# Kernel tuning notes

Hardware: AMD Instinct MI355X
Metric: run time of the kernel (lower is better)

Reference implementation:

```python
import jax, jax.numpy as jnp
import numpy as np

DIM = 512
HEADS = 8
ALPHA = 0.5
HIDDEN = int(DIM * 2.0)
EPS = 1e-5


def _layernorm(x, g, b):
    mu = jnp.mean(x, axis=-1, keepdims=True)
    var = jnp.var(x, axis=-1, keepdims=True)
    return (x - mu) * jax.lax.rsqrt(var + EPS) * g + b


def setup_inputs() -> dict:
    key = jax.random.key(0)
    ks = jax.random.split(key, 8)
    B, N, C = 4, 1536, DIM
    s = lambda fan_in: 1.0 / np.sqrt(fan_in)
    return {
        "x": jax.random.normal(ks[0], (B, N, C), dtype=jnp.float32),
        "ln1_g": jnp.ones((C,), jnp.float32),
        "ln1_b": jnp.zeros((C,), jnp.float32),
        "qkv_w": jax.random.normal(ks[1], (C, 3 * C), jnp.float32) * s(C),
        "qkv_b": jnp.zeros((3 * C,), jnp.float32),
        "ln2_g": jnp.ones((C,), jnp.float32),
        "ln2_b": jnp.zeros((C,), jnp.float32),
        "fc1_w": jax.random.normal(ks[2], (C, HIDDEN), jnp.float32) * s(C),
        "fc1_b": jnp.zeros((HIDDEN,), jnp.float32),
        "fc2_w": jax.random.normal(ks[3], (HIDDEN, C), jnp.float32) * s(HIDDEN),
        "fc2_b": jnp.zeros((C,), jnp.float32),
    }


def reference(x, ln1_g, ln1_b, qkv_w, qkv_b, ln2_g, ln2_b, fc1_w, fc1_b, fc2_w, fc2_b):
    B, N, C = x.shape
    H = HEADS
    d = C // H
    S = N // 3

    h = _layernorm(x, ln1_g, ln1_b)
    qkv = (h @ qkv_w + qkv_b).reshape(B, N, 3, H, d)
    qkv = jnp.transpose(qkv, (2, 0, 3, 1, 4))  # [3,B,H,N,d]
    q, k, v = qkv[0], qkv[1], qkv[2]

    attn = jnp.einsum('bhnd,bhmd->bhnm', q, k) * (d ** -0.5)  # [B,H,N,N]
    # sequential cross-segment score mixing (matches in-place torch semantics)
    s0 = attn[:, :, 0:S]
    s1 = attn[:, :, S:2 * S] + ALPHA * s0
    s2 = attn[:, :, 2 * S:] + ALPHA * s1
    attn = jnp.concatenate([s0, s1, s2], axis=2)
    attn = jax.nn.softmax(attn, axis=-1)

    o = jnp.einsum('bhnm,bhmd->bhnd', attn, v)
    o = jnp.transpose(o, (0, 2, 1, 3)).reshape(B, N, C)
    x = x + o  # NOTE: self.proj is defined but unused in the original forward

    h2 = _layernorm(x, ln2_g, ln2_b)
    m = jax.nn.gelu(h2 @ fc1_w + fc1_b, approximate=False) @ fc2_w + fc2_b
    return x + m
```

## Files before the change

kernel.cpp:

```cpp
#include <hip/hip_runtime.h>
#include <hip/hip_bf16.h>
#include <math.h>

#define DIMC 512
#define NSEQ 1536
#define BATCH 4
#define NHEADS 8
#define HDIM 64
#define SSEG 512
#define HIDDEN_DIM 1024
#define ALPHA_C 0.5f
#define EPS_C 1e-5f
#define NROWS (BATCH*NSEQ)
#define SHIFT_L2 8.65617025f
#define QSCALE_L2 0.18033688f

typedef __attribute__((ext_vector_type(8))) short bfrag8;
typedef __attribute__((ext_vector_type(8))) _Float16 hfrag8;
typedef __attribute__((ext_vector_type(2))) __fp16 h2;
typedef __attribute__((ext_vector_type(4))) float ffrag;
typedef float4 f4;

__device__ __forceinline__ ushort f2bf(float v) {
    __hip_bfloat16 hb = __float2bfloat16(v);
    return *(ushort*)&hb;
}

__device__ __forceinline__ void gl2lds16(const ushort* g, ushort* l) {
    __builtin_amdgcn_global_load_lds(
        (const __attribute__((address_space(1))) unsigned*)g,
        (__attribute__((address_space(3))) unsigned*)l, 16, 0, 0);
}

__global__ __launch_bounds__(256)
void prep_kernel(const float* __restrict__ qkv_w, const float* __restrict__ fc1_w,
                 const float* __restrict__ fc2_w, ushort* __restrict__ qkv_wt,
                 ushort* __restrict__ fc1_wt, ushort* __restrict__ fc2_wt,
                 const float* __restrict__ x, const float* __restrict__ g,
                 const float* __restrict__ bvec, ushort* __restrict__ h_out)
{
    int bid = blockIdx.x;
    if (bid < 448) {
        __shared__ float tile[64][65];
        const float* W; ushort* Wt; int K, N, n0, k0;
        if (bid < 192)      { W = qkv_w; Wt = qkv_wt; K = 512;  N = 1536; int b = bid;       n0 = (b % 24) * 64; k0 = (b / 24) * 64; }
        else if (bid < 320) { W = fc1_w; Wt = fc1_wt; K = 512;  N = 1024; int b = bid - 192; n0 = (b % 16) * 64; k0 = (b / 16) * 64; }
        else                { W = fc2_w; Wt = fc2_wt; K = 1024; N = 512;  int b = bid - 320; n0 = (b % 8)  * 64; k0 = (b / 8)  * 64; }
        int tx = threadIdx.x & 63, ty = threadIdx.x >> 6;
        #pragma unroll
        for (int i = 0; i < 16; i++) {
            int r = i * 4 + ty;
            tile[r][tx] = W[(size_t)(k0 + r) * N + n0 + tx];
        }
        __syncthreads();
        #pragma unroll
        for (int i = 0; i < 16; i++) {
            int r = i * 4 + ty;
            Wt[(size_t)(n0 + r) * K + k0 + tx] = f2bf(tile[tx][r]);
        }
    } else {
        __shared__ float red[16];
        int row = bid - 448;
        int t = threadIdx.x;
        int lane = t & 63, w = t >> 6;
        const float* rp = x + (size_t)row * DIMC;
        float v0 = rp[t];
        float v1 = rp[t + 256];
        float s = v0 + v1;
        float s2 = v0 * v0 + v1 * v1;
        #pragma unroll
        for (int o = 32; o > 0; o >>= 1) {
            s  += __shfl_down(s,  o, 64);
            s2 += __shfl_down(s2, o, 64);
        }
        if (lane == 0) { red[w] = s; red[8 + w] = s2; }
        __syncthreads();
        if (t == 0) {
            float a = red[0] + red[1] + red[2] + red[3];
            float c = red[8] + red[9] + red[10] + red[11];
            red[0] = a; red[8] = c;
        }
        __syncthreads();
        float mean = red[0] * (1.0f / DIMC);
        float var  = red[8] * (1.0f / DIMC) - mean * mean;
        float rstd = rsqrtf(var + EPS_C);
        ushort* op = h_out + (size_t)row * DIMC;
        op[t]       = f2bf((v0 - mean) * rstd * g[t]       + bvec[t]);
        op[t + 256] = f2bf((v1 - mean) * rstd * g[t + 256] + bvec[t + 256]);
    }
}

__global__ __launch_bounds__(256)
void ln_kernel(const float* __restrict__ in, const float* __restrict__ g,
               const float* __restrict__ b, ushort* __restrict__ out)
{
    __shared__ float red[16];
    int row = blockIdx.x;
    int t = threadIdx.x;
    int lane = t & 63, w = t >> 6;
    const float* rp = in + (size_t)row * DIMC;
    float v0 = rp[t];
    float v1 = rp[t + 256];
    float s = v0 + v1;
    float s2 = v0 * v0 + v1 * v1;
    #pragma unroll
    for (int o = 32; o > 0; o >>= 1) {
        s  += __shfl_down(s,  o, 64);
        s2 += __shfl_down(s2, o, 64);
    }
    if (lane == 0) { red[w] = s; red[8 + w] = s2; }
    __syncthreads();
    if (t == 0) {
        float a = red[0] + red[1] + red[2] + red[3];
        float c = red[8] + red[9] + red[10] + red[11];
        red[0] = a; red[8] = c;
    }
    __syncthreads();
    float mean = red[0] * (1.0f / DIMC);
    float var  = red[8] * (1.0f / DIMC) - mean * mean;
    float rstd = rsqrtf(var + EPS_C);
    ushort* op = out + (size_t)row * DIMC;
    op[t]       = f2bf((v0 - mean) * rstd * g[t]       + b[t]);
    op[t + 256] = f2bf((v1 - mean) * rstd * g[t + 256] + b[t + 256]);
}

template <int EPI>
__device__ __forceinline__
void mgemm_body(const ushort* __restrict__ A, const ushort* __restrict__ Wt,
                const float* __restrict__ bias, const float* resid,
                void* out, int M, int K, int Nn, int bx, int by,
                ushort* As, ushort* Bs)
{
    int tid = threadIdx.x;
    int lane = tid & 63, w = tid >> 6;
    int cl = lane & 15, qg = lane >> 4;
    int wm = w >> 1, wn = w & 1;
    int rowBase = by * 64, colBase = bx * 64;
    int sr = lane >> 2;
    int sb = (lane & 3) * 8;

    const ushort* agb = A  + (size_t)(rowBase + w * 16 + sr) * K + sb;
    const ushort* bgb = Wt + (size_t)(colBase + w * 16 + sr) * K + sb;

    ffrag acc[2][2];
    #pragma unroll
    for (int mi = 0; mi < 2; mi++)
        #pragma unroll
        for (int ni = 0; ni < 2; ni++)
            #pragma unroll
            for (int r = 0; r < 4; r++) acc[mi][ni][r] = 0.f;

    int niter = K >> 6;

    #pragma unroll
    for (int hf = 0; hf < 2; hf++) {
        gl2lds16(agb + hf * 32, As + (0 * 2 + hf) * 2048 + (w * 16) * 32);
        gl2lds16(bgb + hf * 32, Bs + (0 * 2 + hf) * 2048 + (w * 16) * 32);
    }
    __syncthreads();

    for (int it = 0; it < niter; it++) {
        int cur = it & 1;
        if (it + 1 < niter) {
            int k0 = (it + 1) * 64;
            #pragma unroll
            for (int hf = 0; hf < 2; hf++) {
                gl2lds16(agb + k0 + hf * 32, As + ((cur ^ 1) * 2 + hf) * 2048 + (w * 16) * 32);
                gl2lds16(bgb + k0 + hf * 32, Bs + ((cur ^ 1) * 2 + hf) * 2048 + (w * 16) * 32);
            }
        }
        #pragma unroll
        for (int ks = 0; ks < 2; ks++) {
            bfrag8 af[2], bf[2];
            #pragma unroll
            for (int mi = 0; mi < 2; mi++)
                af[mi] = *(const bfrag8*)&As[(cur * 2 + ks) * 2048 + (wm * 32 + mi * 16 + cl) * 32 + qg * 8];
            #pragma unroll
            for (int ni = 0; ni < 2; ni++)
                bf[ni] = *(const bfrag8*)&Bs[(cur * 2 + ks) * 2048 + (wn * 32 + ni * 16 + cl) * 32 + qg * 8];
            #pragma unroll
            for (int mi = 0; mi < 2; mi++)
                #pragma unroll
                for (int ni = 0; ni < 2; ni++)
                    acc[mi][ni] = __builtin_amdgcn_mfma_f32_16x16x32_bf16(af[mi], bf[ni], acc[mi][ni], 0, 0, 0);
        }
        if (it + 1 < niter) __syncthreads();
    }

    #pragma unroll
    for (int mi = 0; mi < 2; mi++) {
        #pragma unroll
        for (int ni = 0; ni < 2; ni++) {
            #pragma unroll
            for (int r = 0; r < 4; r++) {
                int row = rowBase + wm * 32 + mi * 16 + qg * 4 + r;
                int col = colBase + wn * 32 + ni * 16 + cl;
                float v = acc[mi][ni][r] + (EPI == 3 ? bias[row] : bias[col]);
                if (EPI == 0 && col < DIMC) v *= QSCALE_L2;
                if (EPI == 1) v = 0.5f * v * (1.0f + erff(v * 0.70710678118654752f));
                if (EPI == 2) {
                    v += resid[(size_t)row * Nn + col];
                    ((float*)out)[(size_t)row * Nn + col] = v;
                } else if (EPI == 3) {
                    _Float16 e = (_Float16)v;
                    int t = col & 31;
                    int pcol = (col & ~31) | (((t & 15) >> 2) * 8 + (t >> 4) * 4 + (t & 3));
                    ((ushort*)out)[(size_t)row * Nn + pcol] = *(ushort*)&e;
                } else {
                    ((ushort*)out)[(size_t)row * Nn + col] = f2bf(v);
                }
            }
        }
    }
}

template <int EPI>
__device__ __forceinline__
void mgemm128_body(const ushort* __restrict__ A, const ushort* __restrict__ Wt,
                   const float* __restrict__ bias, void* out,
                   int K, int Nn, int bx, int by,
                   ushort* As, ushort* Bs)
{
    int tid = threadIdx.x;
    int lane = tid & 63, w = tid >> 6;
    int cl = lane & 15, qg = lane >> 4;
    int wm = w >> 1, wn = w & 1;
    int rowBase = by * 64, colBase = bx * 128;
    int sr = lane >> 2;
    int sb = (lane & 3) * 8;

    const ushort* agb = A  + (size_t)(rowBase + w * 16 + sr) * K + sb;
    const ushort* bgb = Wt + (size_t)(colBase + w * 32 + sr) * K + sb;

    ffrag acc[2][4];
    #pragma unroll
    for (int mi = 0; mi < 2; mi++)
        #pragma unroll
        for (int ni = 0; ni < 4; ni++)
            #pragma unroll
            for (int r = 0; r < 4; r++) acc[mi][ni][r] = 0.f;

    int niter = K >> 6;

    #pragma unroll
    for (int hf = 0; hf < 2; hf++) {
        gl2lds16(agb + hf * 32,                  As + (0 * 2 + hf) * 2048 + (w * 16) * 32);
        gl2lds16(bgb + hf * 32,                  Bs + (0 * 2 + hf) * 4096 + (w * 32) * 32);
        gl2lds16(bgb + (size_t)16 * K + hf * 32, Bs + (0 * 2 + hf) * 4096 + (w * 32 + 16) * 32);
    }
    __syncthreads();

    for (int it = 0; it < niter; it++) {
        int cur = it & 1;
        if (it + 1 < niter) {
            int k0 = (it + 1) * 64;
            #pragma unroll
            for (int hf = 0; hf < 2; hf++) {
                gl2lds16(agb + k0 + hf * 32,                  As + ((cur ^ 1) * 2 + hf) * 2048 + (w * 16) * 32);
                gl2lds16(bgb + k0 + hf * 32,                  Bs + ((cur ^ 1) * 2 + hf) * 4096 + (w * 32) * 32);
                gl2lds16(bgb + (size_t)16 * K + k0 + hf * 32, Bs + ((cur ^ 1) * 2 + hf) * 4096 + (w * 32 + 16) * 32);
            }
        }
        #pragma unroll
        for (int ks = 0; ks < 2; ks++) {
            bfrag8 af[2], bf[4];
            #pragma unroll
            for (int mi = 0; mi < 2; mi++)
                af[mi] = *(const bfrag8*)&As[(cur * 2 + ks) * 2048 + (wm * 32 + mi * 16 + cl) * 32 + qg * 8];
            #pragma unroll
            for (int ni = 0; ni < 4; ni++)
                bf[ni] = *(const bfrag8*)&Bs[(cur * 2 + ks) * 4096 + (wn * 64 + ni * 16 + cl) * 32 + qg * 8];
            #pragma unroll
            for (int mi = 0; mi < 2; mi++)
                #pragma unroll
                for (int ni = 0; ni < 4; ni++)
                    acc[mi][ni] = __builtin_amdgcn_mfma_f32_16x16x32_bf16(af[mi], bf[ni], acc[mi][ni], 0, 0, 0);
        }
        if (it + 1 < niter) __syncthreads();
    }

    #pragma unroll
    for (int mi = 0; mi < 2; mi++) {
        #pragma unroll
        for (int ni = 0; ni < 4; ni++) {
            #pragma unroll
            for (int r = 0; r < 4; r++) {
                int row = rowBase + wm * 32 + mi * 16 + qg * 4 + r;
                int col = colBase + wn * 64 + ni * 16 + cl;
                float v = acc[mi][ni][r] + bias[col];
                if (EPI == 0 && col < DIMC) v *= QSCALE_L2;
                if (EPI == 1) v = 0.5f * v * (1.0f + erff(v * 0.70710678118654752f));
                ((ushort*)out)[(size_t)row * Nn + col] = f2bf(v);
            }
        }
    }
}

template <int EPI>
__global__ __launch_bounds__(256)
void mgemm_kernel(const ushort* __restrict__ A, const ushort* __restrict__ Wt,
                  const float* __restrict__ bias, const float* resid,
                  void* out, int M, int K, int Nn)
{
    __shared__ ushort As[2 * 2 * 64 * 32];
    __shared__ ushort Bs[2 * 2 * 64 * 32];
    mgemm_body<EPI>(A, Wt, bias, resid, out, M, K, Nn, blockIdx.x, blockIdx.y, As, Bs);
}

template <int EPI>
__global__ __launch_bounds__(256)
void mgemm128_kernel(const ushort* __restrict__ A, const ushort* __restrict__ Wt,
                     const float* __restrict__ bias, void* out, int K, int Nn)
{
    __shared__ ushort As[2 * 2 * 64 * 32];
    __shared__ ushort Bs[2 * 2 * 128 * 32];
    mgemm128_body<EPI>(A, Wt, bias, out, K, Nn, blockIdx.x, blockIdx.y, As, Bs);
}

__global__ __launch_bounds__(256)
void qkvt_kernel(const ushort* __restrict__ h_bf, const ushort* __restrict__ qkv_wt,
                 const float* __restrict__ qkv_b, ushort* __restrict__ qkb,
                 ushort* __restrict__ vtb)
{
    __shared__ ushort smem[2 * 2 * 192 * 32];
    int bid = blockIdx.x;
    if (bid < 768) {
        mgemm128_body<0>(h_bf, qkv_wt, qkv_b, (void*)qkb,
                         DIMC, 2 * DIMC, bid & 7, bid >> 3,
                         smem, smem + 2 * 2 * 64 * 32);
    } else {
        int b2 = bid - 768;
        mgemm_body<3>(qkv_wt + (size_t)2 * DIMC * DIMC, h_bf, qkv_b + 2 * DIMC, nullptr,
                      (void*)vtb, DIMC, DIMC, NROWS, b2 % 96, b2 / 96,
                      smem, smem + 2 * 2 * 64 * 32);
    }
}

__global__ __launch_bounds__(256)
void attn_kernel(const ushort* __restrict__ qk, const ushort* __restrict__ vt,
                 const float* __restrict__ x, float* __restrict__ xres)
{
    __shared__ float Op[48][68];
    __shared__ float Lp[4][4][16][3];

    int n = blockIdx.x + (blockIdx.y << 5);
    int idx = n >> 3;
    int bh  = (n & 7) * 4 + (idx & 3);
    int qi0 = (idx >> 2) * 16;
    int b = bh >> 3, h = bh & 7;
    int tid = threadIdx.x;
    int lane = tid & 63, w = tid >> 6;
    int cl = lane & 15, qg = lane >> 4;

    const ushort* base = qk + (size_t)b * NSEQ * 1024 + h * HDIM;
    const _Float16* vbase = (const _Float16*)vt + (size_t)(h * HDIM) * NROWS + b * NSEQ;

    bfrag8 bq[3][2];
    #pragma unroll
    for (int seg = 0; seg < 3; seg++)
        #pragma unroll
        for (int f = 0; f < 2; f++)
            bq[seg][f] = *(const bfrag8*)(base + (size_t)(seg * SSEG + qi0 + cl) * 1024 + f * 32 + qg * 8);

    ffrag o[3][4];
    #pragma unroll
    for (int seg = 0; seg < 3; seg++)
        #pragma unroll
        for (int mg = 0; mg < 4; mg++)
            #pragma unroll
            for (int r = 0; r < 4; r++) o[seg][mg][r] = 0.f;
    float lp[3] = {0.f, 0.f, 0.f};

    int kb = w * 384;

    const _Float16* vp[4];
    #pragma unroll
    for (int mg = 0; mg < 4; mg++)
        vp[mg] = vbase + (size_t)(mg * 16 + cl) * NROWS + kb + qg * 8;
    const ushort* kp[2][2];
    #pragma unroll
    for (int s = 0; s < 2; s++)
        #pragma unroll
        for (int f = 0; f < 2; f++)
            kp[s][f] = base + (size_t)(kb + s * 16 + cl) * 1024 + 512 + f * 32 + qg * 8;

    auto loadf = [&](hfrag8* av, bfrag8 (*af)[2]) {
        #pragma unroll
        for (int mg = 0; mg < 4; mg++) {
            av[mg] = *(const hfrag8*)vp[mg];
            vp[mg] += 32;
        }
        #pragma unroll
        for (int s = 0; s < 2; s++)
            #pragma unroll
            for (int f = 0; f < 2; f++) {
                af[s][f] = *(const bfrag8*)kp[s][f];
                kp[s][f] += 32 * 1024;
            }
    };

    auto comp = [&](const hfrag8* av, const bfrag8 (*af)[2]) {
        ffrag c[2][3];
        #pragma unroll
        for (int s = 0; s < 2; s++) {
            #pragma unroll
            for (int seg = 0; seg < 3; seg++) {
                #pragma unroll
                for (int r = 0; r < 4; r++) c[s][seg][r] = 0.f;
                c[s][seg] = __builtin_amdgcn_mfma_f32_16x16x32_bf16(af[s][0], bq[seg][0], c[s][seg], 0, 0, 0);
                c[s][seg] = __builtin_amdgcn_mfma_f32_16x16x32_bf16(af[s][1], bq[seg][1], c[s][seg], 0, 0, 0);
            }
        }
        #pragma unroll
        for (int s = 0; s < 2; s++) {
            #pragma unroll
            for (int r = 0; r < 4; r++) {
                float s0 = c[s][0][r];
                float s1 = c[s][1][r] + ALPHA_C * s0;
                float s2 = c[s][2][r] + ALPHA_C * s1;
                float e0 = __builtin_amdgcn_exp2f(s0 - SHIFT_L2);
                float e1 = __builtin_amdgcn_exp2f(s1 - SHIFT_L2);
                float e2 = __builtin_amdgcn_exp2f(s2 - SHIFT_L2);
                c[s][0][r] = e0; c[s][1][r] = e1; c[s][2][r] = e2;
                lp[0] += e0; lp[1] += e1; lp[2] += e2;
            }
        }
        #pragma unroll
        for (int seg = 0; seg < 3; seg++) {
            union { hfrag8 v8; h2 v2[4]; } u;
            u.v2[0] = __builtin_amdgcn_cvt_pkrtz(c[0][seg][0], c[0][seg][1]);
            u.v2[1] = __builtin_amdgcn_cvt_pkrtz(c[0][seg][2], c[0][seg][3]);
            u.v2[2] = __builtin_amdgcn_cvt_pkrtz(c[1][seg][0], c[1][seg][1]);
            u.v2[3] = __builtin_amdgcn_cvt_pkrtz(c[1][seg][2], c[1][seg][3]);
            #pragma unroll
            for (int mg = 0; mg < 4; mg++)
                o[seg][mg] = __builtin_amdgcn_mfma_f32_16x16x32_f16(av[mg], u.v8, o[seg][mg], 0, 0, 0);
        }
    };

    hfrag8 avA[4], avB[4];
    bfrag8 afA[2][2], afB[2][2];
    loadf(avA, afA);
    #pragma unroll 1
    for (int it = 0; it < 12; it += 2) {
        loadf(avB, afB);
        comp(avA, afA);
        if (it + 2 < 12) loadf(avA, afA);
        comp(avB, afB);
    }

    #pragma unroll
    for (int seg = 0; seg < 3; seg++) Lp[w][qg][cl][seg] = lp[seg];

    #pragma unroll 1
    for (int wv = 0; wv < 4; wv++) {
        __syncthreads();
        if (w == wv) {
            #pragma unroll
            for (int seg = 0; seg < 3; seg++)
                #pragma unroll
                for (int mg = 0; mg < 4; mg++) {
                    float* dst = &Op[seg * 16 + cl][mg * 16 + qg * 4];
                    if (wv == 0) {
                        #pragma unroll
                        for (int r = 0; r < 4; r++) dst[r] = o[seg][mg][r];
                    } else {
                        #pragma unroll
                        for (int r = 0; r < 4; r++) dst[r] += o[seg][mg][r];
                    }
                }
        }
    }
    __syncthreads();

    if (tid < 192) {
        int row = tid >> 2;
        int seg = row >> 4, q16 = row & 15;
        int d0 = (tid & 3) * 16;
        float l = 0.f;
        #pragma unroll
        for (int wv = 0; wv < 4; wv++)
            #pragma unroll
            for (int g2 = 0; g2 < 4; g2++)
                l += Lp[wv][g2][q16][seg];
        float invl = 1.0f / l;
        size_t rowg = ((size_t)(b * NSEQ + seg * SSEG + qi0 + q16)) * DIMC + h * HDIM + d0;
        #pragma unroll
        for (int dd = 0; dd < 16; dd += 4) {
            f4 xv = *(const f4*)(x + rowg + dd);
            f4 ov;
            ov.x = Op[row][d0 + dd + 0] * invl + xv.x;
            ov.y = Op[row][d0 + dd + 1] * invl + xv.y;
            ov.z = Op[row][d0 + dd + 2] * invl + xv.z;
            ov.w = Op[row][d0 + dd + 3] * invl + xv.w;
            *(f4*)(xres + rowg + dd) = ov;
        }
    }
}

extern "C" void kernel_launch(void* const* d_in, const int* in_sizes, int n_in,
                              void* d_out, int out_size, void* d_ws, size_t ws_size,
                              hipStream_t stream)
{
    const float* x     = (const float*)d_in[0];
    const float* ln1_g = (const float*)d_in[1];
    const float* ln1_b = (const float*)d_in[2];
    const float* qkv_w = (const float*)d_in[3];
    const float* qkv_b = (const float*)d_in[4];
    const float* ln2_g = (const float*)d_in[5];
    const float* ln2_b = (const float*)d_in[6];
    const float* fc1_w = (const float*)d_in[7];
    const float* fc1_b = (const float*)d_in[8];
    const float* fc2_w = (const float*)d_in[9];
    const float* fc2_b = (const float*)d_in[10];
    float* out = (float*)d_out;

    char* p = (char*)d_ws;
    ushort* h_bf    = (ushort*)p;  p += (size_t)NROWS * DIMC * 2;
    ushort* qkb     = (ushort*)p;  p += (size_t)NROWS * 2 * DIMC * 2;
    ushort* vtb     = (ushort*)p;  p += (size_t)DIMC * NROWS * 2;
    ushort* mid     = (ushort*)p;  p += (size_t)NROWS * HIDDEN_DIM * 2;
    ushort* qkv_wt  = (ushort*)p;  p += (size_t)3 * DIMC * DIMC * 2;
    ushort* fc1_wt  = (ushort*)p;  p += (size_t)HIDDEN_DIM * DIMC * 2;
    ushort* fc2_wt  = (ushort*)p;
    float* xres = out;

    prep_kernel<<<448 + NROWS, 256, 0, stream>>>(qkv_w, fc1_w, fc2_w, qkv_wt, fc1_wt, fc2_wt,
                                                 x, ln1_g, ln1_b, h_bf);

    qkvt_kernel<<<1536, 256, 0, stream>>>(h_bf, qkv_wt, qkv_b, qkb, vtb);

    attn_kernel<<<dim3(SSEG / 16, BATCH * NHEADS), 256, 0, stream>>>(qkb, vtb, x, xres);

    ln_kernel<<<NROWS, 256, 0, stream>>>(xres, ln2_g, ln2_b, h_bf);

    mgemm128_kernel<1><<<dim3(HIDDEN_DIM / 128, NROWS / 64), 256, 0, stream>>>(
        h_bf, fc1_wt, fc1_b, (void*)mid, DIMC, HIDDEN_DIM);

    mgemm_kernel<2><<<dim3(DIMC / 64, NROWS / 64), 256, 0, stream>>>(
        mid, fc2_wt, fc2_b, xres, (void*)out, NROWS, HIDDEN_DIM, DIMC);
}
```

Baseline: 210.2 us.

## Store Q, K, V in fragment-packed per-head tiles for contiguous attention loads

The QKV GEMM epilogue now scatters Q, K and V into per-(batch,head) blocked layouts that match the MFMA fragment order. The attention kernel then reads each fragment from contiguous 1-2 KB chunks instead of strided rows 1024 or NROWS elements apart. This is meant to cut memory transactions and TLB/cache pressure in the attention inner loop. In exchange, the GEMM epilogue writes become more scattered, and address arithmetic is added on both sides.

```diff
diff --git a/kernel.cpp b/kernel.cpp
--- a/kernel.cpp
+++ b/kernel.cpp
@@ -21,6 +21,7 @@
 typedef __attribute__((ext_vector_type(4))) float ffrag;
 typedef float4 f4;
 
+
 __device__ __forceinline__ ushort f2bf(float v) {
     __hip_bfloat16 hb = __float2bfloat16(v);
     return *(ushort*)&hb;
@@ -187,6 +188,8 @@
         if (it + 1 < niter) __syncthreads();
     }
 
+    int bb = (EPI == 3) ? (colBase / 1536) : 0;
+
     #pragma unroll
     for (int mi = 0; mi < 2; mi++) {
         #pragma unroll
@@ -202,10 +205,14 @@
                     v += resid[(size_t)row * Nn + col];
                     ((float*)out)[(size_t)row * Nn + col] = v;
                 } else if (EPI == 3) {
+                    int t = col - bb * 1536;
+                    int h = row >> 6, dl = row & 63;
+                    int t32 = t & 31;
+                    int slot = ((t32 & 15) >> 2) * 8 + (t32 >> 4) * 4 + (t32 & 3);
+                    size_t a = ((size_t)(bb * 8 + h) * 48 + (t >> 5)) * 2048
+                             + (dl >> 4) * 512 + (dl & 15) * 32 + slot;
                     _Float16 e = (_Float16)v;
-                    int t = col & 31;
-                    int pcol = (col & ~31) | (((t & 15) >> 2) * 8 + (t >> 4) * 4 + (t & 3));
-                    ((ushort*)out)[(size_t)row * Nn + pcol] = *(ushort*)&e;
+                    ((ushort*)out)[a] = *(ushort*)&e;
                 } else {
                     ((ushort*)out)[(size_t)row * Nn + col] = f2bf(v);
                 }
@@ -217,7 +224,7 @@
 template <int EPI>
 __device__ __forceinline__
 void mgemm128_body(const ushort* __restrict__ A, const ushort* __restrict__ Wt,
-                   const float* __restrict__ bias, void* out,
+                   const float* __restrict__ bias, void* out, void* out2,
                    int K, int Nn, int bx, int by,
                    ushort* As, ushort* Bs)
 {
@@ -279,6 +286,8 @@
         if (it + 1 < niter) __syncthreads();
     }
 
+    int bb = (EPI == 4) ? (rowBase / 1536) : 0;
+
     #pragma unroll
     for (int mi = 0; mi < 2; mi++) {
         #pragma unroll
@@ -288,9 +297,22 @@
                 int row = rowBase + wm * 32 + mi * 16 + qg * 4 + r;
                 int col = colBase + wn * 64 + ni * 16 + cl;
                 float v = acc[mi][ni][r] + bias[col];
-                if (EPI == 0 && col < DIMC) v *= QSCALE_L2;
-                if (EPI == 1) v = 0.5f * v * (1.0f + erff(v * 0.70710678118654752f));
-                ((ushort*)out)[(size_t)row * Nn + col] = f2bf(v);
+                if (EPI == 1) {
+                    v = 0.5f * v * (1.0f + erff(v * 0.70710678118654752f));
+                    ((ushort*)out)[(size_t)row * Nn + col] = f2bf(v);
+                } else if (EPI == 4) {
+                    int t = row - bb * 1536;
+                    int h = (col >> 6) & 7;
+                    int d = col & 63;
+                    size_t a = ((size_t)(bb * 8 + h) * 96 + (t >> 4)) * 1024
+                             + (d >> 5) * 512 + (t & 15) * 32 + (d & 31);
+                    if (col < DIMC) {
+                        v *= QSCALE_L2;
+                        ((ushort*)out)[a] = f2bf(v);
+                    } else {
+                        ((ushort*)out2)[a] = f2bf(v);
+                    }
+                }
             }
         }
     }
@@ -314,30 +336,31 @@
 {
     __shared__ ushort As[2 * 2 * 64 * 32];
     __shared__ ushort Bs[2 * 2 * 128 * 32];
-    mgemm128_body<EPI>(A, Wt, bias, out, K, Nn, blockIdx.x, blockIdx.y, As, Bs);
+    mgemm128_body<EPI>(A, Wt, bias, out, nullptr, K, Nn, blockIdx.x, blockIdx.y, As, Bs);
 }
 
 __global__ __launch_bounds__(256)
 void qkvt_kernel(const ushort* __restrict__ h_bf, const ushort* __restrict__ qkv_wt,
-                 const float* __restrict__ qkv_b, ushort* __restrict__ qkb,
-                 ushort* __restrict__ vtb)
+                 const float* __restrict__ qkv_b, ushort* __restrict__ qpk,
+                 ushort* __restrict__ kpk, ushort* __restrict__ vpk)
 {
     __shared__ ushort smem[2 * 2 * 192 * 32];
     int bid = blockIdx.x;
     if (bid < 768) {
-        mgemm128_body<0>(h_bf, qkv_wt, qkv_b, (void*)qkb,
+        mgemm128_body<4>(h_bf, qkv_wt, qkv_b, (void*)qpk, (void*)kpk,
                          DIMC, 2 * DIMC, bid & 7, bid >> 3,
                          smem, smem + 2 * 2 * 64 * 32);
     } else {
         int b2 = bid - 768;
         mgemm_body<3>(qkv_wt + (size_t)2 * DIMC * DIMC, h_bf, qkv_b + 2 * DIMC, nullptr,
-                      (void*)vtb, DIMC, DIMC, NROWS, b2 % 96, b2 / 96,
+                      (void*)vpk, DIMC, DIMC, NROWS, b2 % 96, b2 / 96,
                       smem, smem + 2 * 2 * 64 * 32);
     }
 }
 
 __global__ __launch_bounds__(256)
-void attn_kernel(const ushort* __restrict__ qk, const ushort* __restrict__ vt,
+void attn_kernel(const ushort* __restrict__ qpk, const ushort* __restrict__ kpk,
+                 const ushort* __restrict__ vpk,
                  const float* __restrict__ x, float* __restrict__ xres)
 {
     __shared__ float Op[48][68];
@@ -352,15 +375,17 @@
     int lane = tid & 63, w = tid >> 6;
     int cl = lane & 15, qg = lane >> 4;
 
-    const ushort* base = qk + (size_t)b * NSEQ * 1024 + h * HDIM;
-    const _Float16* vbase = (const _Float16*)vt + (size_t)(h * HDIM) * NROWS + b * NSEQ;
+    int lofs = cl * 32 + qg * 8;
+    const ushort* qb = qpk + (size_t)bh * 96 * 1024;
+    const ushort* kb = kpk + (size_t)bh * 96 * 1024;
+    const ushort* vb = vpk + (size_t)bh * 48 * 2048;
 
     bfrag8 bq[3][2];
     #pragma unroll
     for (int seg = 0; seg < 3; seg++)
         #pragma unroll
         for (int f = 0; f < 2; f++)
-            bq[seg][f] = *(const bfrag8*)(base + (size_t)(seg * SSEG + qi0 + cl) * 1024 + f * 32 + qg * 8);
+            bq[seg][f] = *(const bfrag8*)&qb[(size_t)((seg * SSEG + qi0) >> 4) * 1024 + f * 512 + lofs];
 
     ffrag o[3][4];
     #pragma unroll
@@ -371,32 +396,22 @@
             for (int r = 0; r < 4; r++) o[seg][mg][r] = 0.f;
     float lp[3] = {0.f, 0.f, 0.f};
 
-    int kb = w * 384;
-
-    const _Float16* vp[4];
-    #pragma unroll
-    for (int mg = 0; mg < 4; mg++)
-        vp[mg] = vbase + (size_t)(mg * 16 + cl) * NROWS + kb + qg * 8;
-    const ushort* kp[2][2];
-    #pragma unroll
-    for (int s = 0; s < 2; s++)
-        #pragma unroll
-        for (int f = 0; f < 2; f++)
-            kp[s][f] = base + (size_t)(kb + s * 16 + cl) * 1024 + 512 + f * 32 + qg * 8;
+    int kb0 = w * 384;
+
+    const ushort* kptr = kb + (size_t)(kb0 >> 4) * 1024 + lofs;
+    const ushort* vptr = vb + (size_t)(kb0 >> 5) * 2048 + lofs;
 
     auto loadf = [&](hfrag8* av, bfrag8 (*af)[2]) {
         #pragma unroll
-        for (int mg = 0; mg < 4; mg++) {
-            av[mg] = *(const hfrag8*)vp[mg];
-            vp[mg] += 32;
-        }
+        for (int mg = 0; mg < 4; mg++)
+            av[mg] = *(const hfrag8*)(vptr + mg * 512);
+        vptr += 2048;
         #pragma unroll
         for (int s = 0; s < 2; s++)
             #pragma unroll
-            for (int f = 0; f < 2; f++) {
-                af[s][f] = *(const bfrag8*)kp[s][f];
-                kp[s][f] += 32 * 1024;
-            }
+            for (int f = 0; f < 2; f++)
+                af[s][f] = *(const bfrag8*)(kptr + s * 1024 + f * 512);
+        kptr += 2048;
     };
 
     auto comp = [&](const hfrag8* av, const bfrag8 (*af)[2]) {
@@ -517,8 +532,9 @@
 
     char* p = (char*)d_ws;
     ushort* h_bf    = (ushort*)p;  p += (size_t)NROWS * DIMC * 2;
-    ushort* qkb     = (ushort*)p;  p += (size_t)NROWS * 2 * DIMC * 2;
-    ushort* vtb     = (ushort*)p;  p += (size_t)DIMC * NROWS * 2;
+    ushort* qpk     = (ushort*)p;  p += (size_t)32 * 96 * 1024 * 2;
+    ushort* kpk     = (ushort*)p;  p += (size_t)32 * 96 * 1024 * 2;
+    ushort* vpk     = (ushort*)p;  p += (size_t)32 * 48 * 2048 * 2;
     ushort* mid     = (ushort*)p;  p += (size_t)NROWS * HIDDEN_DIM * 2;
     ushort* qkv_wt  = (ushort*)p;  p += (size_t)3 * DIMC * DIMC * 2;
     ushort* fc1_wt  = (ushort*)p;  p += (size_t)HIDDEN_DIM * DIMC * 2;
@@ -528,9 +544,9 @@
     prep_kernel<<<448 + NROWS, 256, 0, stream>>>(qkv_w, fc1_w, fc2_w, qkv_wt, fc1_wt, fc2_wt,
                                                  x, ln1_g, ln1_b, h_bf);
 
-    qkvt_kernel<<<1536, 256, 0, stream>>>(h_bf, qkv_wt, qkv_b, qkb, vtb);
-
-    attn_kernel<<<dim3(SSEG / 16, BATCH * NHEADS), 256, 0, stream>>>(qkb, vtb, x, xres);
+    qkvt_kernel<<<1536, 256, 0, stream>>>(h_bf, qkv_wt, qkv_b, qpk, kpk, vpk);
+
+    attn_kernel<<<dim3(SSEG / 16, BATCH * NHEADS), 256, 0, stream>>>(qpk, kpk, vpk, x, xres);
 
     ln_kernel<<<NROWS, 256, 0, stream>>>(xres, ln2_g, ln2_b, h_bf);
 
```

Result: faster. 191.3 us (-9.0%).
